# Kernel optimization log

Hardware: AMD Instinct MI355X
Metric: run time of the kernel (lower is better)

Reference implementation:

```python
import jax, jax.numpy as jnp
import numpy as np

B, N, DF = 8, 4096, 768
K1, K2, DS = 8, 2, 128
KVQ, H, ITERS = 128, 1, 3
DH = KVQ // H
EPS_SA = 1e-8
SCALE = DH ** -0.5


def layer_norm(x, g, b, eps=1e-5):
    m = jnp.mean(x, axis=-1, keepdims=True)
    v = jnp.var(x, axis=-1, keepdims=True)
    return (x - m) / jnp.sqrt(v + eps) * g + b


def gru_cell(x, h, Wih, Whh, bih, bhh):
    gi = x @ Wih.T + bih
    gh = h @ Whh.T + bhh
    ir, iz, inn = jnp.split(gi, 3, axis=-1)
    hr, hz, hn = jnp.split(gh, 3, axis=-1)
    r = jax.nn.sigmoid(ir + hr)
    z = jax.nn.sigmoid(iz + hz)
    n = jnp.tanh(inn + r * hn)
    return (1.0 - z) * n + z * h


def setup_inputs() -> dict:
    key = jax.random.key(0)
    ks = jax.random.split(key, 24)
    s = 0.02
    f32 = jnp.float32
    return {
        'tokens': jax.random.normal(ks[0], (B, N, DF), f32),
        'parent_slots': jax.random.normal(ks[1], (B, K1, DS), f32),
        'parent_masks': jax.random.uniform(ks[2], (B, K1, N), f32),
        'eps_noise': jax.random.normal(ks[3], (B, K1, K2, DS), f32),
        'ln_in_g': jnp.ones((DF,), f32), 'ln_in_b': jnp.zeros((DF,), f32),
        'ln_s_g': jnp.ones((DS,), f32), 'ln_s_b': jnp.zeros((DS,), f32),
        'Wq': jax.random.normal(ks[4], (KVQ, DS), f32) * s,
        'Wk': jax.random.normal(ks[5], (KVQ, DF), f32) * s,
        'Wv': jax.random.normal(ks[6], (KVQ, DF), f32) * s,
        'gru_Wih': jax.random.normal(ks[7], (3 * DS, KVQ), f32) * s,
        'gru_Whh': jax.random.normal(ks[8], (3 * DS, DS), f32) * s,
        'gru_bih': jnp.zeros((3 * DS,), f32),
        'gru_bhh': jnp.zeros((3 * DS,), f32),
        'mlp_ln_g': jnp.ones((DS,), f32), 'mlp_ln_b': jnp.zeros((DS,), f32),
        'mlp_W1': jax.random.normal(ks[9], (4 * DS, DS), f32) * s,
        'mlp_b1': jnp.zeros((4 * DS,), f32),
        'mlp_W2': jax.random.normal(ks[10], (DS, 4 * DS), f32) * s,
        'mlp_b2': jnp.zeros((DS,), f32),
    }


def reference(tokens, parent_slots, parent_masks, eps_noise,
              ln_in_g, ln_in_b, ln_s_g, ln_s_b, Wq, Wk, Wv,
              gru_Wih, gru_Whh, gru_bih, gru_bhh,
              mlp_ln_g, mlp_ln_b, mlp_W1, mlp_b1, mlp_W2, mlp_b2):
    BK = B * K1
    # parent-mask gating (all parents vectorized, folded into batch)
    denom = jnp.mean(parent_masks, axis=-1, keepdims=True)          # [B,K1,1]
    safe = (denom > 1e-6).astype(tokens.dtype)
    w_scaled = safe * (parent_masks / (denom + 1e-6)) + (1.0 - safe)  # [B,K1,N]
    tg = (tokens[:, None, :, :] * w_scaled[..., None]).reshape(BK, N, DF)
    slots = (parent_slots[:, :, None, :] + 0.01 * eps_noise).reshape(BK, K2, DS)

    inp = layer_norm(tg, ln_in_g, ln_in_b)
    k = (inp @ Wk.T).reshape(BK, N, H, DH)
    v = (inp @ Wv.T).reshape(BK, N, H, DH)

    attn_bw = None
    for _ in range(ITERS):
        slots_prev = slots
        sn = layer_norm(slots, ln_s_g, ln_s_b)
        q = (sn @ Wq.T).reshape(BK, K2, H, DH)
        dots = jnp.einsum('bihd,bjhd->bihj', q, k) * SCALE          # [BK,K2,H,N]
        attn = jax.nn.softmax(dots, axis=1) + EPS_SA                # softmax over slots
        attn_bw = attn
        attn_w = attn / jnp.sum(attn, axis=-1, keepdims=True)
        updates = jnp.einsum('bjhd,bihj->bihd', v, attn_w).reshape(BK * K2, KVQ)
        slots = gru_cell(updates, slots_prev.reshape(BK * K2, DS),
                         gru_Wih, gru_Whh, gru_bih, gru_bhh).reshape(BK, K2, DS)
        h = layer_norm(slots, mlp_ln_g, mlp_ln_b)
        slots = jax.nn.gelu(h @ mlp_W1.T + mlp_b1, approximate=False) @ mlp_W2.T + mlp_b2

    attn_out = jnp.mean(attn_bw, axis=2)                            # [BK,K2,N]
    child_objects = slots.reshape(B, K1 * K2, DS)
    child_gating = (attn_out.reshape(B, K1, K2, N) * parent_masks[:, :, None, :]).reshape(B, K1 * K2, N)
    return child_objects, child_gating
```

## Files before the change

kernel.cpp:

```cpp
#include <hip/hip_runtime.h>
#include <hip/hip_bf16.h>
#include <math.h>

#define SCALE_ 0.08838834764831843f

typedef __attribute__((ext_vector_type(8))) short bf16x8;
typedef __attribute__((ext_vector_type(4))) float f32x4;

static const size_t OFF_VAR   = 0;
static const size_t OFF_DENOM = 32768;
static const size_t OFF_BIAS  = 33088;
static const size_t OFF_QKB   = 33344;
static const size_t OFF_SSUM  = 33472;
static const size_t OFF_SLOTS = 33600;
static const size_t OFF_Q     = 49984;
static const size_t OFF_WQBF  = 66368;
static const size_t OFF_WIHBF = 74560;
static const size_t OFF_WHHBF = 99136;
static const size_t OFF_W1BF  = 123712;
static const size_t OFF_WM2BF = 156480;
static const size_t OFF_WKVBF = 189248;
static const size_t OFF_UPART = 287552;
static const size_t OFF_KB    = 1336128;
static const size_t OFF_VT    = 3433280;

__device__ __forceinline__ float wred64(float v) {
#pragma unroll
  for (int off = 32; off > 0; off >>= 1) v += __shfl_xor(v, off, 64);
  return v;
}

__device__ __forceinline__ unsigned short f2bf(float f) {
  unsigned u = __float_as_uint(f);
  unsigned r = (u + 0x7fffu + ((u >> 16) & 1u)) >> 16;
  return (unsigned short)r;
}

__device__ __forceinline__ unsigned pack2(float a, float b) {
  float2 f; f.x = a; f.y = b;
  __hip_bfloat162 h = __float22bfloat162_rn(f);
  unsigned r;
  __builtin_memcpy(&r, &h, 4);
  return r;
}

__global__ __launch_bounds__(256) void prep_all_k(
    const float* __restrict__ Wk, const float* __restrict__ Wv,
    const float* __restrict__ g, const float* __restrict__ bb,
    const float* __restrict__ Wq, const float* __restrict__ Wih,
    const float* __restrict__ Whh, const float* __restrict__ W1,
    const float* __restrict__ W2, const float* __restrict__ pm,
    unsigned short* __restrict__ wkv, float* __restrict__ biasArr,
    unsigned short* __restrict__ Wqbf, unsigned short* __restrict__ Wihbf,
    unsigned short* __restrict__ Whhbf, unsigned short* __restrict__ W1bf,
    unsigned short* __restrict__ Wm2bf, float* __restrict__ denomArr)
{
  __shared__ float red4[4];
  int bi = blockIdx.x, t = threadIdx.x;
  if (bi < 64) {
    int j = bi*4 + (t >> 6), lane = t & 63;
    const float* w = (j < 128) ? (Wk + (size_t)j*768) : (Wv + (size_t)(j-128)*768);
    float gs = 0.f, bs = 0.f;
    float st[12];
    int key = j & 7;
#pragma unroll
    for (int s = 0; s < 12; ++s) {
      int dd = lane + s*64;
      float wv = w[dd], gv = g[dd];
      st[s] = wv*gv;
      gs += st[s]; bs += bb[dd]*wv;
    }
    gs = wred64(gs); bs = wred64(bs);
    float corr = gs*(1.f/768.f);
#pragma unroll
    for (int s = 0; s < 12; ++s) {
      int dd = lane + s*64;
      int sw = (dd & ~63) | (((((dd >> 3) & 7) ^ key)) << 3) | (dd & 7);
      wkv[(size_t)j*768 + sw] = f2bf(st[s] - corr);
    }
    if (lane == 0) biasArr[j] = bs;
  } else if (bi < 128) {
    int idx = (bi-64)*256 + t;  Wqbf[idx]  = f2bf(Wq[idx]);
  } else if (bi < 320) {
    int idx = (bi-128)*256 + t; Wihbf[idx] = f2bf(Wih[idx]);
  } else if (bi < 512) {
    int idx = (bi-320)*256 + t; Whhbf[idx] = f2bf(Whh[idx]);
  } else if (bi < 768) {
    int idx = (bi-512)*256 + t; W1bf[idx]  = f2bf(W1[idx]);
  } else if (bi < 1024) {
    int idx = (bi-768)*256 + t; Wm2bf[idx] = f2bf(W2[idx]);
  } else {
    int bk = bi - 1024;
    float s = 0.f;
#pragma unroll
    for (int k = 0; k < 16; ++k) s += pm[bk*4096 + t + k*256];
    s = wred64(s);
    if ((t & 63) == 0) red4[t >> 6] = s;
    __syncthreads();
    if (t == 0) denomArr[bk] = (red4[0]+red4[1]+red4[2]+red4[3])*(1.f/4096.f);
  }
}

__global__ __launch_bounds__(256) void gemm_kv_k(
    const float* __restrict__ tokens, const unsigned short* __restrict__ wkv,
    unsigned short* __restrict__ Kb, unsigned short* __restrict__ VT,
    float* __restrict__ varArr)
{
  __shared__ unsigned short As[64*64];
  __shared__ unsigned short Bs[128*64];
  int bi = blockIdx.x;
  int jb = bi & 1;
  int r0 = (bi >> 1)*64;
  int t = threadIdx.x;
  int w = t >> 6, lane = t & 63;
  int lm = lane & 15, lq = lane >> 4;
  int g16 = t >> 4, seg = t & 15;
  int m0 = (w >> 1)*32, n0 = (w & 1)*64;
  const unsigned short* wsrc = wkv + (size_t)jb*128*768;

  f32x4 acc[2][4];
#pragma unroll
  for (int a = 0; a < 2; ++a)
#pragma unroll
    for (int c = 0; c < 4; ++c) acc[a][c] = f32x4{0.f, 0.f, 0.f, 0.f};
  float s1[4] = {0.f,0.f,0.f,0.f}, s2[4] = {0.f,0.f,0.f,0.f};

  for (int k0 = 0; k0 < 768; k0 += 64) {
    __syncthreads();
#pragma unroll
    for (int s = 0; s < 4; ++s) {
      int row = w*32 + s*8;
      __builtin_amdgcn_global_load_lds(
        (const __attribute__((address_space(1))) void*)
          (wsrc + (size_t)(row + (lane >> 3))*768 + k0 + (lane & 7)*8),
        (__attribute__((address_space(3))) void*)(&Bs[row*64]), 16, 0, 0);
    }
#pragma unroll
    for (int p = 0; p < 4; ++p) {
      int row = p*16 + g16;
      float4 x = *(const float4*)(tokens + (size_t)(r0 + row)*768 + k0 + seg*4);
      s1[p] += x.x + x.y + x.z + x.w;
      s2[p] += x.x*x.x + x.y*x.y + x.z*x.z + x.w*x.w;
      int off = row*64 + (((seg >> 1) ^ (row & 7)) << 3) + (seg & 1)*4;
      *(uint2*)(&As[off]) = make_uint2(pack2(x.x, x.y), pack2(x.z, x.w));
    }
    __syncthreads();
#pragma unroll
    for (int kk8 = 0; kk8 < 8; kk8 += 4) {
      bf16x8 af[2], bfr[4];
#pragma unroll
      for (int mt = 0; mt < 2; ++mt) {
        int row = m0 + mt*16 + lm;
        af[mt] = *(const bf16x8*)(&As[row*64 + (((kk8 + lq) ^ (row & 7)) << 3)]);
      }
#pragma unroll
      for (int nt = 0; nt < 4; ++nt) {
        int row = n0 + nt*16 + lm;
        bfr[nt] = *(const bf16x8*)(&Bs[row*64 + (((kk8 + lq) ^ (row & 7)) << 3)]);
      }
#pragma unroll
      for (int mt = 0; mt < 2; ++mt)
#pragma unroll
        for (int nt = 0; nt < 4; ++nt)
          acc[mt][nt] = __builtin_amdgcn_mfma_f32_16x16x32_bf16(
              af[mt], bfr[nt], acc[mt][nt], 0, 0, 0);
    }
  }
#pragma unroll
  for (int p = 0; p < 4; ++p) {
#pragma unroll
    for (int m = 8; m >= 1; m >>= 1) {
      s1[p] += __shfl_xor(s1[p], m, 16);
      s2[p] += __shfl_xor(s2[p], m, 16);
    }
  }
  if (jb == 0 && seg == 0) {
#pragma unroll
    for (int p = 0; p < 4; ++p) {
      int row = p*16 + g16;
      float m = s1[p]*(1.f/768.f);
      varArr[r0 + row] = s2[p]*(1.f/768.f) - m*m;
    }
  }
  if (jb == 0) {
#pragma unroll
    for (int nt = 0; nt < 4; ++nt) {
      int col = n0 + nt*16 + lm;
#pragma unroll
      for (int mt = 0; mt < 2; ++mt) {
#pragma unroll
        for (int reg = 0; reg < 4; ++reg) {
          int tok = r0 + m0 + mt*16 + lq*4 + reg;
          Kb[(size_t)tok*128 + col] = f2bf(acc[mt][nt][reg]);
        }
      }
    }
  } else {
#pragma unroll
    for (int nt = 0; nt < 4; ++nt) {
      int d = n0 + nt*16 + lm;
#pragma unroll
      for (int mt = 0; mt < 2; ++mt) {
        int tok0 = r0 + m0 + mt*16 + lq*4;
        int b = tok0 >> 12;
        int n = tok0 & 4095;
        uint2 v = make_uint2(pack2(acc[mt][nt][0], acc[mt][nt][1]),
                             pack2(acc[mt][nt][2], acc[mt][nt][3]));
        *(uint2*)&VT[((size_t)(b*128 + d))*4096 + n] = v;
      }
    }
  }
}

__global__ __launch_bounds__(256, 1) void slots_init_q_k(
    const float* __restrict__ ps, const float* __restrict__ eps,
    const float* __restrict__ g_s, const float* __restrict__ b_s,
    const unsigned short* __restrict__ Wqbf, const float* __restrict__ biasArr,
    float* __restrict__ slots, float* __restrict__ qg, float* __restrict__ qkb,
    float* __restrict__ Ssum)
{
  __shared__ unsigned short Fsn[2048];
  __shared__ float qkbL[16];
  int R0 = blockIdx.x*16;
  int t = threadIdx.x;
  int w = t >> 6, ln = t & 63, lm = ln & 15, lq = ln >> 4;
  if (t < 16) qkbL[t] = 0.f;
  {
    int r = t >> 4, dseg = t & 15, ds8 = dseg*8;
    int row = R0 + r, bk = row >> 1;
    float xv[8]; float s1 = 0.f, s2 = 0.f;
#pragma unroll
    for (int j = 0; j < 8; ++j) {
      int d = ds8 + j;
      float x = ps[bk*128 + d] + 0.01f*eps[row*128 + d];
      slots[row*128 + d] = x;
      xv[j] = x; s1 += x; s2 += x*x;
    }
#pragma unroll
    for (int m = 8; m >= 1; m >>= 1) {
      s1 += __shfl_xor(s1, m, 16);
      s2 += __shfl_xor(s2, m, 16);
    }
    float mean = s1*(1.f/128.f);
    float var = s2*(1.f/128.f) - mean*mean;
    float rstd = rsqrtf(var + 1e-5f);
    float sv[8];
#pragma unroll
    for (int j = 0; j < 8; ++j) {
      int d = ds8 + j;
      sv[j] = (xv[j] - mean)*rstd*g_s[d] + b_s[d];
    }
    int fa = ((dseg >> 2)*64 + (dseg & 3)*16 + r)*8;
    *(uint4*)&Fsn[fa] = make_uint4(pack2(sv[0],sv[1]), pack2(sv[2],sv[3]),
                                   pack2(sv[4],sv[5]), pack2(sv[6],sv[7]));
  }
  __syncthreads();
  {
    bf16x8 af[4];
#pragma unroll
    for (int kc = 0; kc < 4; ++kc)
      af[kc] = *(const bf16x8*)(&Fsn[(kc*64 + ln)*8]);
    float pr[4] = {0.f, 0.f, 0.f, 0.f};
#pragma unroll
    for (int i = 0; i < 2; ++i) {
      int n0 = w*32 + i*16;
      f32x4 acc = f32x4{0.f,0.f,0.f,0.f};
#pragma unroll
      for (int kc = 0; kc < 4; ++kc) {
        bf16x8 bw = *(const bf16x8*)(&Wqbf[(size_t)(n0+lm)*128 + kc*32 + lq*8]);
        acc = __builtin_amdgcn_mfma_f32_16x16x32_bf16(af[kc], bw, acc, 0,0,0);
      }
      int n = n0 + lm;
      float bk_ = biasArr[n];
#pragma unroll
      for (int reg = 0; reg < 4; ++reg) {
        int row = lq*4 + reg;
        qg[(size_t)(R0 + row)*128 + n] = acc[reg];
        pr[reg] += acc[reg]*bk_;
      }
    }
#pragma unroll
    for (int reg = 0; reg < 4; ++reg) {
#pragma unroll
      for (int m = 8; m >= 1; m >>= 1) pr[reg] += __shfl_xor(pr[reg], m, 16);
    }
    if (lm == 0) {
#pragma unroll
      for (int reg = 0; reg < 4; ++reg)
        atomicAdd(&qkbL[lq*4 + reg], pr[reg]);
    }
  }
  __syncthreads();
  if (t < 16) { qkb[R0 + t] = qkbL[t]; Ssum[R0 + t] = 0.f; }
}

__global__ __launch_bounds__(128) void attn_fused_k(
    const unsigned short* __restrict__ Kb, const unsigned short* __restrict__ VT,
    const float* __restrict__ qg, const float* __restrict__ qkb,
    const float* __restrict__ varArr, const float* __restrict__ denomArr,
    const float* __restrict__ pm,
    float* __restrict__ Upart, float* __restrict__ Ssum,
    float* __restrict__ outG, int last)
{
  __shared__ unsigned short Pl[2][16*68];
  __shared__ float Upw[2][2048];
  int bi = blockIdx.x;
  int b = bi >> 5, nch = bi & 31;
  int t = threadIdx.x;
  int wv = t >> 6, ln = t & 63;
  int lm = ln & 15, lq = ln >> 4;
  int ntok0 = nch*128 + wv*64;
  unsigned short* pl = &Pl[wv][0];

  bf16x8 qf[4];
#pragma unroll
  for (int kc = 0; kc < 4; ++kc) {
    const float* qp = qg + (size_t)(b*16 + lm)*128 + kc*32 + lq*8;
    float4 q0 = *(const float4*)qp;
    float4 q1 = *(const float4*)(qp + 4);
    uint4 tmp = make_uint4(pack2(q0.x,q0.y), pack2(q0.z,q0.w),
                           pack2(q1.x,q1.y), pack2(q1.z,q1.w));
    qf[kc] = *(bf16x8*)&tmp;
  }
  float qkbv[4];
#pragma unroll
  for (int reg = 0; reg < 4; ++reg) qkbv[reg] = qkb[b*16 + lq*4 + reg];
  float den0 = denomArr[b*8 + lq*2];
  float den1 = denomArr[b*8 + lq*2 + 1];
  bool g0 = den0 > 1e-6f, g1 = den1 > 1e-6f;
  float inv0 = 1.f/(den0 + 1e-6f), inv1 = 1.f/(den1 + 1e-6f);

  f32x4 Uacc[8];
#pragma unroll
  for (int dt = 0; dt < 8; ++dt) Uacc[dt] = f32x4{0.f,0.f,0.f,0.f};
  float sAcc[4] = {0.f, 0.f, 0.f, 0.f};

#pragma unroll
  for (int half = 0; half < 2; ++half) {
    int tk0 = ntok0 + half*32;
#pragma unroll
    for (int ti = 0; ti < 2; ++ti) {
      int n0 = tk0 + ti*16;
      int n = n0 + lm;
      f32x4 dacc = f32x4{0.f,0.f,0.f,0.f};
      const unsigned short* kp = Kb + ((size_t)(b*4096 + n))*128 + lq*8;
#pragma unroll
      for (int kc = 0; kc < 4; ++kc) {
        bf16x8 kf = *(const bf16x8*)(kp + kc*32);
        dacc = __builtin_amdgcn_mfma_f32_16x16x32_bf16(qf[kc], kf, dacc, 0,0,0);
      }
      float vv = varArr[b*4096 + n];
      float pm0 = pm[((size_t)(b*8 + lq*2))*4096 + n];
      float pm1 = pm[((size_t)(b*8 + lq*2 + 1))*4096 + n];
      float c0 = g0 ? pm0*inv0 : 1.f;
      float c1 = g1 ? pm1*inv1 : 1.f;
      float al0 = c0*rsqrtf(c0*c0*vv + 1e-5f);
      float al1 = c1*rsqrtf(c1*c1*vv + 1e-5f);
      float dd0 = SCALE_*(al0*dacc[0] + qkbv[0]);
      float dd1 = SCALE_*(al0*dacc[1] + qkbv[1]);
      float mx0 = fmaxf(dd0, dd1);
      float e0 = expf(dd0 - mx0), e1 = expf(dd1 - mx0);
      float is0 = 1.f/(e0 + e1);
      float o0 = e0*is0 + 1e-8f, o1 = e1*is0 + 1e-8f;
      float dd2 = SCALE_*(al1*dacc[2] + qkbv[2]);
      float dd3 = SCALE_*(al1*dacc[3] + qkbv[3]);
      float mx1 = fmaxf(dd2, dd3);
      float e2 = expf(dd2 - mx1), e3 = expf(dd3 - mx1);
      float is1 = 1.f/(e2 + e3);
      float o2 = e2*is1 + 1e-8f, o3 = e3*is1 + 1e-8f;
      sAcc[0] += o0; sAcc[1] += o1; sAcc[2] += o2; sAcc[3] += o3;
      if (last) {
        size_t ob = ((size_t)(b*16 + lq*4))*4096 + n;
        outG[ob]          = o0*pm0;
        outG[ob + 4096]   = o1*pm0;
        outG[ob + 8192]   = o2*pm1;
        outG[ob + 12288]  = o3*pm1;
      }
      int pc = half*32 + ti*16 + lm;
      pl[(lq*4 + 0)*68 + pc] = f2bf(o0*al0);
      pl[(lq*4 + 1)*68 + pc] = f2bf(o1*al0);
      pl[(lq*4 + 2)*68 + pc] = f2bf(o2*al1);
      pl[(lq*4 + 3)*68 + pc] = f2bf(o3*al1);
    }
    bf16x8 pf = *(const bf16x8*)&pl[lm*68 + half*32 + lq*8];
    const unsigned short* vp = VT + ((size_t)(b*128 + lm))*4096 + tk0 + lq*8;
#pragma unroll
    for (int dt = 0; dt < 8; ++dt) {
      bf16x8 vf = *(const bf16x8*)(vp + (size_t)(dt*16)*4096);
      Uacc[dt] = __builtin_amdgcn_mfma_f32_16x16x32_bf16(pf, vf, Uacc[dt], 0,0,0);
    }
  }

#pragma unroll
  for (int reg = 0; reg < 4; ++reg) {
    float r = sAcc[reg];
    r += __shfl_xor(r, 1, 64); r += __shfl_xor(r, 2, 64);
    r += __shfl_xor(r, 4, 64); r += __shfl_xor(r, 8, 64);
    if (lm == 0) atomicAdd(&Ssum[b*16 + lq*4 + reg], r);
  }
  float* uw = &Upw[wv][0];
#pragma unroll
  for (int dt = 0; dt < 8; ++dt)
#pragma unroll
    for (int reg = 0; reg < 4; ++reg)
      uw[(lq*4 + reg)*128 + dt*16 + lm] = Uacc[dt][reg];
  __syncthreads();
  float* up = Upart + (size_t)(b*32 + nch)*2048;
#pragma unroll
  for (int i = 0; i < 4; ++i) {
    int idx = t*16 + i*4;
    float4 a = *(const float4*)&Upw[0][idx];
    float4 c = *(const float4*)&Upw[1][idx];
    float4 o; o.x = a.x + c.x; o.y = a.y + c.y; o.z = a.z + c.z; o.w = a.w + c.w;
    *(float4*)&up[idx] = o;
  }
}

__global__ __launch_bounds__(256, 1) void gru_mlp_q_k(
    const float* __restrict__ Upart, const float* __restrict__ Ssum,
    const float* __restrict__ biasArr,
    const unsigned short* __restrict__ Wihbf, const unsigned short* __restrict__ Whhbf,
    const float* __restrict__ bih, const float* __restrict__ bhh,
    const float* __restrict__ mlp_g, const float* __restrict__ mlp_b,
    const unsigned short* __restrict__ W1bf, const float* __restrict__ b1,
    const unsigned short* __restrict__ Wm2bf, const float* __restrict__ b2,
    const float* __restrict__ ln_s_g, const float* __restrict__ ln_s_b,
    const unsigned short* __restrict__ Wqbf,
    float* __restrict__ slots, float* __restrict__ qg, float* __restrict__ qkb,
    float* __restrict__ SsumW, float* __restrict__ outObj, int last)
{
  __shared__ unsigned short FXx[2048], FXh[2048], Fhn[2048], Fsn[2048];
  __shared__ unsigned short Ft1[8192];
  __shared__ float G_rz[16*256];
  __shared__ float G_in[16*128];
  __shared__ float G_hn[16*128];
  __shared__ float hs_[16*128];
  __shared__ float os_[16*128];
  __shared__ float qkbL[16];

  int R0 = blockIdx.x*16;
  int t = threadIdx.x;
  int w = t >> 6, ln = t & 63;
  int lm = ln & 15, lq = ln >> 4;

  {
    int r = t >> 4, dseg = t & 15, ds8 = dseg*8;
    int R = R0 + r;
    float ua[8];
#pragma unroll
    for (int j = 0; j < 8; ++j) ua[j] = 0.f;
    const float* up = Upart + (size_t)blockIdx.x*65536 + r*128 + ds8;
#pragma unroll 8
    for (int ch = 0; ch < 32; ++ch) {
      float4 u0 = *(const float4*)(up + (size_t)ch*2048);
      float4 u1 = *(const float4*)(up + (size_t)ch*2048 + 4);
      ua[0]+=u0.x; ua[1]+=u0.y; ua[2]+=u0.z; ua[3]+=u0.w;
      ua[4]+=u1.x; ua[5]+=u1.y; ua[6]+=u1.z; ua[7]+=u1.w;
    }
    float Sv = 1.f/Ssum[R];
    float4 bv0 = *(const float4*)(biasArr + 128 + ds8);
    float4 bv1 = *(const float4*)(biasArr + 132 + ds8);
    float xv[8];
    xv[0]=ua[0]*Sv+bv0.x; xv[1]=ua[1]*Sv+bv0.y; xv[2]=ua[2]*Sv+bv0.z; xv[3]=ua[3]*Sv+bv0.w;
    xv[4]=ua[4]*Sv+bv1.x; xv[5]=ua[5]*Sv+bv1.y; xv[6]=ua[6]*Sv+bv1.z; xv[7]=ua[7]*Sv+bv1.w;
    float4 h0 = *(const float4*)(slots + (size_t)R*128 + ds8);
    float4 h1 = *(const float4*)(slots + (size_t)R*128 + ds8 + 4);
    *(float4*)(hs_ + r*128 + ds8) = h0;
    *(float4*)(hs_ + r*128 + ds8 + 4) = h1;
    int fa = ((dseg >> 2)*64 + (dseg & 3)*16 + r)*8;
    *(uint4*)&FXx[fa] = make_uint4(pack2(xv[0],xv[1]), pack2(xv[2],xv[3]),
                                   pack2(xv[4],xv[5]), pack2(xv[6],xv[7]));
    *(uint4*)&FXh[fa] = make_uint4(pack2(h0.x,h0.y), pack2(h0.z,h0.w),
                                   pack2(h1.x,h1.y), pack2(h1.z,h1.w));
    if (t < 16) qkbL[t] = 0.f;
  }
  __syncthreads();

  {
    bf16x8 ax[4], ah[4];
#pragma unroll
    for (int kc = 0; kc < 4; ++kc) {
      ax[kc] = *(const bf16x8*)(&FXx[(kc*64 + ln)*8]);
      ah[kc] = *(const bf16x8*)(&FXh[(kc*64 + ln)*8]);
    }
    if (w < 2) {
#pragma unroll
      for (int i = 0; i < 8; ++i) {
        int n0 = (w*8 + i)*16;
        f32x4 acc = f32x4{0.f,0.f,0.f,0.f};
#pragma unroll
        for (int kc = 0; kc < 4; ++kc) {
          bf16x8 bi_ = *(const bf16x8*)(&Wihbf[(size_t)(n0+lm)*128 + kc*32 + lq*8]);
          acc = __builtin_amdgcn_mfma_f32_16x16x32_bf16(ax[kc], bi_, acc, 0,0,0);
        }
#pragma unroll
        for (int kc = 0; kc < 4; ++kc) {
          bf16x8 bh_ = *(const bf16x8*)(&Whhbf[(size_t)(n0+lm)*128 + kc*32 + lq*8]);
          acc = __builtin_amdgcn_mfma_f32_16x16x32_bf16(ah[kc], bh_, acc, 0,0,0);
        }
#pragma unroll
        for (int reg = 0; reg < 4; ++reg)
          G_rz[(lq*4+reg)*256 + n0 + lm] = acc[reg];
      }
    } else if (w == 2) {
#pragma unroll
      for (int i = 0; i < 8; ++i) {
        int n0 = 256 + i*16;
        f32x4 acc = f32x4{0.f,0.f,0.f,0.f};
#pragma unroll
        for (int kc = 0; kc < 4; ++kc) {
          bf16x8 bi_ = *(const bf16x8*)(&Wihbf[(size_t)(n0+lm)*128 + kc*32 + lq*8]);
          acc = __builtin_amdgcn_mfma_f32_16x16x32_bf16(ax[kc], bi_, acc, 0,0,0);
        }
#pragma unroll
        for (int reg = 0; reg < 4; ++reg)
          G_in[(lq*4+reg)*128 + i*16 + lm] = acc[reg];
      }
    } else {
#pragma unroll
      for (int i = 0; i < 8; ++i) {
        int n0 = 256 + i*16;
        f32x4 acc = f32x4{0.f,0.f,0.f,0.f};
#pragma unroll
        for (int kc = 0; kc < 4; ++kc) {
          bf16x8 bh_ = *(const bf16x8*)(&Whhbf[(size_t)(n0+lm)*128 + kc*32 + lq*8]);
          acc = __builtin_amdgcn_mfma_f32_16x16x32_bf16(ah[kc], bh_, acc, 0,0,0);
        }
#pragma unroll
        for (int reg = 0; reg < 4; ++reg)
          G_hn[(lq*4+reg)*128 + i*16 + lm] = acc[reg];
      }
    }
  }
  __syncthreads();

  {
    int r = t >> 4, dseg = t & 15, ds8 = dseg*8;
    float hp[8];
    float s1 = 0.f, s2 = 0.f;
#pragma unroll
    for (int j = 0; j < 8; ++j) {
      int d = ds8 + j;
      float rg = G_rz[r*256 + d] + bih[d] + bhh[d];
      float zg = G_rz[r*256 + 128 + d] + bih[128+d] + bhh[128+d];
      float ing = G_in[r*128 + d] + bih[256+d];
      float hng = G_hn[r*128 + d] + bhh[256+d];
      float rv = 1.f/(1.f + expf(-rg));
      float zv = 1.f/(1.f + expf(-zg));
      float nv = tanhf(ing + rv*hng);
      float h0 = hs_[r*128 + d];
      float h = (1.f - zv)*nv + zv*h0;
      hp[j] = h;
      s1 += h; s2 += h*h;
    }
#pragma unroll
    for (int m = 8; m >= 1; m >>= 1) {
      s1 += __shfl_xor(s1, m, 16);
      s2 += __shfl_xor(s2, m, 16);
    }
    float mean = s1*(1.f/128.f);
    float var = s2*(1.f/128.f) - mean*mean;
    float rstd = rsqrtf(var + 1e-5f);
    float hv[8];
#pragma unroll
    for (int j = 0; j < 8; ++j) {
      int d = ds8 + j;
      hv[j] = (hp[j] - mean)*rstd*mlp_g[d] + mlp_b[d];
    }
    int fa = ((dseg >> 2)*64 + (dseg & 3)*16 + r)*8;
    *(uint4*)&Fhn[fa] = make_uint4(pack2(hv[0],hv[1]), pack2(hv[2],hv[3]),
                                   pack2(hv[4],hv[5]), pack2(hv[6],hv[7]));
  }
  __syncthreads();

  {
    bf16x8 af[4];
#pragma unroll
    for (int kc = 0; kc < 4; ++kc)
      af[kc] = *(const bf16x8*)(&Fhn[(kc*64 + ln)*8]);
#pragma unroll
    for (int i = 0; i < 8; ++i) {
      int n0 = (w*8 + i)*16;
      f32x4 acc = f32x4{0.f,0.f,0.f,0.f};
#pragma unroll
      for (int kc = 0; kc < 4; ++kc) {
        bf16x8 bw = *(const bf16x8*)(&W1bf[(size_t)(n0+lm)*128 + kc*32 + lq*8]);
        acc = __builtin_amdgcn_mfma_f32_16x16x32_bf16(af[kc], bw, acc, 0,0,0);
      }
      int kdim = n0 + lm;
      float bb = b1[kdim];
      int kc2 = kdim >> 5;
      int sub = (kdim >> 3) & 3;
      int jj = kdim & 7;
#pragma unroll
      for (int reg = 0; reg < 4; ++reg) {
        float v = acc[reg] + bb;
        float gel = 0.5f*v*(1.f + erff(v*0.70710678118654752f));
        Ft1[(kc2*64 + sub*16 + lq*4 + reg)*8 + jj] = f2bf(gel);
      }
    }
  }
  __syncthreads();

  {
#pragma unroll
    for (int i = 0; i < 2; ++i) {
      int n0 = w*32 + i*16;
      f32x4 acc = f32x4{0.f,0.f,0.f,0.f};
#pragma unroll
      for (int kc = 0; kc < 16; ++kc) {
        bf16x8 af = *(const bf16x8*)(&Ft1[(kc*64 + ln)*8]);
        bf16x8 bw = *(const bf16x8*)(&Wm2bf[(size_t)(n0+lm)*512 + kc*32 + lq*8]);
        acc = __builtin_amdgcn_mfma_f32_16x16x32_bf16(af, bw, acc, 0,0,0);
      }
      int n = n0 + lm;
      float bb = b2[n];
#pragma unroll
      for (int reg = 0; reg < 4; ++reg) {
        int row = lq*4 + reg;
        float o = acc[reg] + bb;
        slots[(size_t)(R0 + row)*128 + n] = o;
        os_[row*128 + n] = o;
        if (last) outObj[(size_t)(R0 + row)*128 + n] = o;
      }
    }
  }

  if (last) return;

  __syncthreads();
  {
    int r = t >> 4, dseg = t & 15, ds8 = dseg*8;
    float ov[8];
    float s1 = 0.f, s2 = 0.f;
#pragma unroll
    for (int j = 0; j < 8; ++j) {
      float o = os_[r*128 + ds8 + j];
      ov[j] = o; s1 += o; s2 += o*o;
    }
#pragma unroll
    for (int m = 8; m >= 1; m >>= 1) {
      s1 += __shfl_xor(s1, m, 16);
      s2 += __shfl_xor(s2, m, 16);
    }
    float mean = s1*(1.f/128.f);
    float var = s2*(1.f/128.f) - mean*mean;
    float rstd = rsqrtf(var + 1e-5f);
    float sv[8];
#pragma unroll
    for (int j = 0; j < 8; ++j) {
      int d = ds8 + j;
      sv[j] = (ov[j] - mean)*rstd*ln_s_g[d] + ln_s_b[d];
    }
    int fa = ((dseg >> 2)*64 + (dseg & 3)*16 + r)*8;
    *(uint4*)&Fsn[fa] = make_uint4(pack2(sv[0],sv[1]), pack2(sv[2],sv[3]),
                                   pack2(sv[4],sv[5]), pack2(sv[6],sv[7]));
  }
  __syncthreads();

  {
    bf16x8 af[4];
#pragma unroll
    for (int kc = 0; kc < 4; ++kc)
      af[kc] = *(const bf16x8*)(&Fsn[(kc*64 + ln)*8]);
    float pr[4] = {0.f, 0.f, 0.f, 0.f};
#pragma unroll
    for (int i = 0; i < 2; ++i) {
      int n0 = w*32 + i*16;
      f32x4 acc = f32x4{0.f,0.f,0.f,0.f};
#pragma unroll
      for (int kc = 0; kc < 4; ++kc) {
        bf16x8 bw = *(const bf16x8*)(&Wqbf[(size_t)(n0+lm)*128 + kc*32 + lq*8]);
        acc = __builtin_amdgcn_mfma_f32_16x16x32_bf16(af[kc], bw, acc, 0,0,0);
      }
      int n = n0 + lm;
      float bk_ = biasArr[n];
#pragma unroll
      for (int reg = 0; reg < 4; ++reg) {
        int row = lq*4 + reg;
        qg[(size_t)(R0 + row)*128 + n] = acc[reg];
        pr[reg] += acc[reg]*bk_;
      }
    }
#pragma unroll
    for (int reg = 0; reg < 4; ++reg) {
#pragma unroll
      for (int m = 8; m >= 1; m >>= 1) pr[reg] += __shfl_xor(pr[reg], m, 16);
    }
    if (lm == 0) {
#pragma unroll
      for (int reg = 0; reg < 4; ++reg)
        atomicAdd(&qkbL[lq*4 + reg], pr[reg]);
    }
  }
  __syncthreads();
  if (t < 16) {
    qkb[R0 + t] = qkbL[t];
    SsumW[R0 + t] = 0.f;
  }
}

extern "C" void kernel_launch(void* const* d_in, const int* in_sizes, int n_in,
                              void* d_out, int out_size, void* d_ws, size_t ws_size,
                              hipStream_t stream) {
  const float* tokens = (const float*)d_in[0];
  const float* pslots = (const float*)d_in[1];
  const float* pmasks = (const float*)d_in[2];
  const float* eps    = (const float*)d_in[3];
  const float* ln_in_g= (const float*)d_in[4];
  const float* ln_in_b= (const float*)d_in[5];
  const float* ln_s_g = (const float*)d_in[6];
  const float* ln_s_b = (const float*)d_in[7];
  const float* Wq     = (const float*)d_in[8];
  const float* Wk     = (const float*)d_in[9];
  const float* Wv     = (const float*)d_in[10];
  const float* Wih    = (const float*)d_in[11];
  const float* Whh    = (const float*)d_in[12];
  const float* bih    = (const float*)d_in[13];
  const float* bhh    = (const float*)d_in[14];
  const float* mlp_g  = (const float*)d_in[15];
  const float* mlp_b  = (const float*)d_in[16];
  const float* W1     = (const float*)d_in[17];
  const float* b1     = (const float*)d_in[18];
  const float* W2     = (const float*)d_in[19];
  const float* b2     = (const float*)d_in[20];
  float* ws  = (float*)d_ws;
  float* out = (float*)d_out;
  unsigned short* wkvbf = (unsigned short*)(ws + OFF_WKVBF);
  unsigned short* wqbf  = (unsigned short*)(ws + OFF_WQBF);
  unsigned short* wihbf = (unsigned short*)(ws + OFF_WIHBF);
  unsigned short* whhbf = (unsigned short*)(ws + OFF_WHHBF);
  unsigned short* w1bf  = (unsigned short*)(ws + OFF_W1BF);
  unsigned short* wm2bf = (unsigned short*)(ws + OFF_WM2BF);
  unsigned short* kb    = (unsigned short*)(ws + OFF_KB);
  unsigned short* vt    = (unsigned short*)(ws + OFF_VT);

  prep_all_k<<<1088, 256, 0, stream>>>(Wk, Wv, ln_in_g, ln_in_b,
                                       Wq, Wih, Whh, W1, W2, pmasks,
                                       wkvbf, ws + OFF_BIAS,
                                       wqbf, wihbf, whhbf, w1bf, wm2bf,
                                       ws + OFF_DENOM);
  gemm_kv_k<<<1024, 256, 0, stream>>>(tokens, wkvbf, kb, vt, ws + OFF_VAR);
  slots_init_q_k<<<8, 256, 0, stream>>>(pslots, eps, ln_s_g, ln_s_b,
                                        wqbf, ws + OFF_BIAS,
                                        ws + OFF_SLOTS, ws + OFF_Q,
                                        ws + OFF_QKB, ws + OFF_SSUM);
  for (int it = 0; it < 3; ++it) {
    int last = (it == 2);
    attn_fused_k<<<256, 128, 0, stream>>>(kb, vt, ws + OFF_Q, ws + OFF_QKB,
                                          ws + OFF_VAR, ws + OFF_DENOM, pmasks,
                                          ws + OFF_UPART, ws + OFF_SSUM,
                                          out + 16384, last);
    gru_mlp_q_k<<<8, 256, 0, stream>>>(ws + OFF_UPART, ws + OFF_SSUM,
                                       ws + OFF_BIAS, wihbf, whhbf, bih, bhh,
                                       mlp_g, mlp_b, w1bf, b1, wm2bf, b2,
                                       ln_s_g, ln_s_b, wqbf,
                                       ws + OFF_SLOTS, ws + OFF_Q, ws + OFF_QKB,
                                       ws + OFF_SSUM, out, last);
  }
}
```

Measured before the change: 333.6 us.

## Double-buffer weight tiles and load token A fragments directly to registers in KV GEMM

```diff
diff --git a/kernel.cpp b/kernel.cpp
--- a/kernel.cpp
+++ b/kernel.cpp
@@ -106,110 +106,98 @@
     unsigned short* __restrict__ Kb, unsigned short* __restrict__ VT,
     float* __restrict__ varArr)
 {
-  __shared__ unsigned short As[64*64];
-  __shared__ unsigned short Bs[128*64];
+  __shared__ unsigned short Bs[2][128*128];
   int bi = blockIdx.x;
   int jb = bi & 1;
   int r0 = (bi >> 1)*64;
   int t = threadIdx.x;
   int w = t >> 6, lane = t & 63;
   int lm = lane & 15, lq = lane >> 4;
-  int g16 = t >> 4, seg = t & 15;
-  int m0 = (w >> 1)*32, n0 = (w & 1)*64;
   const unsigned short* wsrc = wkv + (size_t)jb*128*768;
-
-  f32x4 acc[2][4];
-#pragma unroll
-  for (int a = 0; a < 2; ++a)
-#pragma unroll
-    for (int c = 0; c < 4; ++c) acc[a][c] = f32x4{0.f, 0.f, 0.f, 0.f};
-  float s1[4] = {0.f,0.f,0.f,0.f}, s2[4] = {0.f,0.f,0.f,0.f};
-
-  for (int k0 = 0; k0 < 768; k0 += 64) {
-    __syncthreads();
-#pragma unroll
-    for (int s = 0; s < 4; ++s) {
-      int row = w*32 + s*8;
-      __builtin_amdgcn_global_load_lds(
-        (const __attribute__((address_space(1))) void*)
-          (wsrc + (size_t)(row + (lane >> 3))*768 + k0 + (lane & 7)*8),
-        (__attribute__((address_space(3))) void*)(&Bs[row*64]), 16, 0, 0);
-    }
-#pragma unroll
-    for (int p = 0; p < 4; ++p) {
-      int row = p*16 + g16;
-      float4 x = *(const float4*)(tokens + (size_t)(r0 + row)*768 + k0 + seg*4);
-      s1[p] += x.x + x.y + x.z + x.w;
-      s2[p] += x.x*x.x + x.y*x.y + x.z*x.z + x.w*x.w;
-      int off = row*64 + (((seg >> 1) ^ (row & 7)) << 3) + (seg & 1)*4;
-      *(uint2*)(&As[off]) = make_uint2(pack2(x.x, x.y), pack2(x.z, x.w));
-    }
-    __syncthreads();
-#pragma unroll
-    for (int kk8 = 0; kk8 < 8; kk8 += 4) {
-      bf16x8 af[2], bfr[4];
-#pragma unroll
-      for (int mt = 0; mt < 2; ++mt) {
-        int row = m0 + mt*16 + lm;
-        af[mt] = *(const bf16x8*)(&As[row*64 + (((kk8 + lq) ^ (row & 7)) << 3)]);
-      }
-#pragma unroll
-      for (int nt = 0; nt < 4; ++nt) {
-        int row = n0 + nt*16 + lm;
-        bfr[nt] = *(const bf16x8*)(&Bs[row*64 + (((kk8 + lq) ^ (row & 7)) << 3)]);
-      }
-#pragma unroll
-      for (int mt = 0; mt < 2; ++mt)
-#pragma unroll
-        for (int nt = 0; nt < 4; ++nt)
-          acc[mt][nt] = __builtin_amdgcn_mfma_f32_16x16x32_bf16(
-              af[mt], bfr[nt], acc[mt][nt], 0, 0, 0);
-    }
-  }
-#pragma unroll
-  for (int p = 0; p < 4; ++p) {
-#pragma unroll
-    for (int m = 8; m >= 1; m >>= 1) {
-      s1[p] += __shfl_xor(s1[p], m, 16);
-      s2[p] += __shfl_xor(s2[p], m, 16);
-    }
-  }
-  if (jb == 0 && seg == 0) {
-#pragma unroll
-    for (int p = 0; p < 4; ++p) {
-      int row = p*16 + g16;
-      float m = s1[p]*(1.f/768.f);
-      varArr[r0 + row] = s2[p]*(1.f/768.f) - m*m;
-    }
-  }
+  int myrow = r0 + w*16 + lm;
+  const float* arow = tokens + (size_t)myrow*768;
+
+#define DMA9(c, buf) \
+  { int k0_ = (c)*128; \
+    _Pragma("unroll") \
+    for (int s_ = 0; s_ < 8; ++s_) { \
+      int row_ = w*32 + s_*4; \
+      __builtin_amdgcn_global_load_lds( \
+        (const __attribute__((address_space(1))) void*) \
+          (wsrc + (size_t)(row_ + (lane >> 4))*768 + k0_ + (lane & 15)*8), \
+        (__attribute__((address_space(3))) void*)(&Bs[buf][row_*128]), 16, 0, 0); \
+    } }
+
+  f32x4 acc[8];
+#pragma unroll
+  for (int c = 0; c < 8; ++c) acc[c] = f32x4{0.f, 0.f, 0.f, 0.f};
+  float s1 = 0.f, s2 = 0.f;
+
+  DMA9(0, 0);
+  __syncthreads();
+
+  for (int c = 0; c < 6; ++c) {
+    int buf = c & 1;
+    if (c < 5) DMA9(c + 1, buf ^ 1);
+    int k0 = c*128;
+    float4 a[8];
+#pragma unroll
+    for (int ks = 0; ks < 4; ++ks) {
+      a[ks*2]     = *(const float4*)(arow + k0 + ks*32 + lq*8);
+      a[ks*2 + 1] = *(const float4*)(arow + k0 + ks*32 + lq*8 + 4);
+    }
+#pragma unroll
+    for (int ks = 0; ks < 4; ++ks) {
+      float4 x0 = a[ks*2], x1 = a[ks*2 + 1];
+      s1 += x0.x + x0.y + x0.z + x0.w + x1.x + x1.y + x1.z + x1.w;
+      s2 += x0.x*x0.x + x0.y*x0.y + x0.z*x0.z + x0.w*x0.w
+          + x1.x*x1.x + x1.y*x1.y + x1.z*x1.z + x1.w*x1.w;
+      bf16x8 af;
+      { uint4 tmp = make_uint4(pack2(x0.x, x0.y), pack2(x0.z, x0.w),
+                               pack2(x1.x, x1.y), pack2(x1.z, x1.w));
+        af = *(bf16x8*)&tmp; }
+      int q = ks*4 + lq;
+#pragma unroll
+      for (int nt = 0; nt < 8; ++nt) {
+        int row = nt*16 + lm;
+        bf16x8 bfr = *(const bf16x8*)(
+            &Bs[buf][row*128 + (q >> 3)*64 + (((q & 7) ^ (row & 7)) << 3)]);
+        acc[nt] = __builtin_amdgcn_mfma_f32_16x16x32_bf16(af, bfr, acc[nt], 0, 0, 0);
+      }
+    }
+    if (c < 5) __syncthreads();
+  }
+
+  s1 += __shfl_xor(s1, 16, 64); s1 += __shfl_xor(s1, 32, 64);
+  s2 += __shfl_xor(s2, 16, 64); s2 += __shfl_xor(s2, 32, 64);
+  if (jb == 0 && lq == 0) {
+    float m = s1*(1.f/768.f);
+    varArr[myrow] = s2*(1.f/768.f) - m*m;
+  }
+
   if (jb == 0) {
 #pragma unroll
-    for (int nt = 0; nt < 4; ++nt) {
-      int col = n0 + nt*16 + lm;
-#pragma unroll
-      for (int mt = 0; mt < 2; ++mt) {
-#pragma unroll
-        for (int reg = 0; reg < 4; ++reg) {
-          int tok = r0 + m0 + mt*16 + lq*4 + reg;
-          Kb[(size_t)tok*128 + col] = f2bf(acc[mt][nt][reg]);
-        }
+    for (int nt = 0; nt < 8; ++nt) {
+      int col = nt*16 + lm;
+#pragma unroll
+      for (int reg = 0; reg < 4; ++reg) {
+        int tok = r0 + w*16 + lq*4 + reg;
+        Kb[(size_t)tok*128 + col] = f2bf(acc[nt][reg]);
       }
     }
   } else {
 #pragma unroll
-    for (int nt = 0; nt < 4; ++nt) {
-      int d = n0 + nt*16 + lm;
-#pragma unroll
-      for (int mt = 0; mt < 2; ++mt) {
-        int tok0 = r0 + m0 + mt*16 + lq*4;
-        int b = tok0 >> 12;
-        int n = tok0 & 4095;
-        uint2 v = make_uint2(pack2(acc[mt][nt][0], acc[mt][nt][1]),
-                             pack2(acc[mt][nt][2], acc[mt][nt][3]));
-        *(uint2*)&VT[((size_t)(b*128 + d))*4096 + n] = v;
-      }
-    }
-  }
+    for (int nt = 0; nt < 8; ++nt) {
+      int d = nt*16 + lm;
+      int tok0 = r0 + w*16 + lq*4;
+      int b = tok0 >> 12;
+      int n = tok0 & 4095;
+      uint2 v = make_uint2(pack2(acc[nt][0], acc[nt][1]),
+                           pack2(acc[nt][2], acc[nt][3]));
+      *(uint2*)&VT[((size_t)(b*128 + d))*4096 + n] = v;
+    }
+  }
+#undef DMA9
 }
 
 __global__ __launch_bounds__(256, 1) void slots_init_q_k(
```

Result: slower. 356.4 us (+6.9%).
